# Performance work log

Hardware: AMD Instinct MI355X
Metric: run time of the kernel (lower is better)

The kernel has to match this reference:

```python
import jax, jax.numpy as jnp
import numpy as np

OUT_FEATURES = 4096
IN_FEATURES = 4096


def _unpack_int4_symmetric(packed, n_values):
    # packed: uint8-valued int32 array; each byte holds two 4-bit values:
    # high nibble first, low nibble second (packing was (v0 << 4) | v1 with v in [0,15]=q+8)
    high = (packed >> 4) & 15
    low = packed & 15
    interleaved = jnp.stack([high, low], axis=-1).reshape(-1)[:n_values]
    # symmetric: quantized value q = nibble - 8, zero_point = 0
    return interleaved.astype(jnp.float32) - 8.0


def setup_inputs() -> dict:
    key = jax.random.key(0)
    k1, k2, k3, k4, k5 = jax.random.split(key, 5)
    x = jax.random.normal(k1, (4, 2048, IN_FEATURES), dtype=jnp.float32)
    packed_w = jax.random.randint(k2, (OUT_FEATURES * IN_FEATURES // 2,), 0, 256, dtype=jnp.int32)
    packed_b = jax.random.randint(k3, (OUT_FEATURES // 2,), 0, 256, dtype=jnp.int32)
    scale_w = jax.random.uniform(k4, (), dtype=jnp.float32) * 0.01 + 1e-4
    scale_b = jax.random.uniform(k5, (), dtype=jnp.float32) * 0.01 + 1e-4
    return {"x": x, "packed_w": packed_w, "packed_b": packed_b,
            "scale_w": scale_w, "scale_b": scale_b}


def reference(x, packed_w, packed_b, scale_w, scale_b):
    # dequantize weight: scale * (q - zero_point), zero_point = 0 (symmetric)
    qw = _unpack_int4_symmetric(packed_w, OUT_FEATURES * IN_FEATURES)
    W = (scale_w * qw).reshape(OUT_FEATURES, IN_FEATURES)  # [O, I]
    qb = _unpack_int4_symmetric(packed_b, OUT_FEATURES)
    b = scale_b * qb  # [O]
    # F.linear(x, W, b) = x @ W.T + b
    return jnp.einsum('bsi,oi->bso', x, W) + b
```

## Files before the change

kernel.cpp:

```cpp
#include <hip/hip_runtime.h>
#include <hip/hip_bf16.h>

#define M_DIM 8192
#define N_DIM 4096
#define K_DIM 4096

typedef _Float16 f16;
typedef _Float16 f16x8 __attribute__((ext_vector_type(8)));
typedef float f32x16 __attribute__((ext_vector_type(16)));

__device__ __forceinline__ void lds_async16(void* lds, const void* g) {
    __builtin_amdgcn_global_load_lds(
        (const __attribute__((address_space(1))) void*)(void*)g,
        (__attribute__((address_space(3))) void*)lds, 16, 0, 0);
}

__global__ __launch_bounds__(256) void cvt_x_kernel(const float* __restrict__ x, f16* __restrict__ xh) {
    size_t idx  = (size_t)blockIdx.x * 256 + threadIdx.x;
    size_t base = idx * 8;
    const float4* xp = (const float4*)(x + base);
    float4 v0 = xp[0], v1 = xp[1];
    f16x8 h;
    h[0] = (f16)v0.x; h[1] = (f16)v0.y; h[2] = (f16)v0.z; h[3] = (f16)v0.w;
    h[4] = (f16)v1.x; h[5] = (f16)v1.y; h[6] = (f16)v1.z; h[7] = (f16)v1.w;
    *(f16x8*)(xh + base) = h;
}

__global__ __launch_bounds__(256) void cvt_w_kernel(const int* __restrict__ pw, f16* __restrict__ wh) {
    size_t idx = (size_t)blockIdx.x * 256 + threadIdx.x;
    int4 v = ((const int4*)pw)[idx];
    f16x8 h;
    int a;
    a = v.x; h[0] = (f16)(((a >> 4) & 15) - 8); h[1] = (f16)((a & 15) - 8);
    a = v.y; h[2] = (f16)(((a >> 4) & 15) - 8); h[3] = (f16)((a & 15) - 8);
    a = v.z; h[4] = (f16)(((a >> 4) & 15) - 8); h[5] = (f16)((a & 15) - 8);
    a = v.w; h[6] = (f16)(((a >> 4) & 15) - 8); h[7] = (f16)((a & 15) - 8);
    *(f16x8*)(wh + idx * 8) = h;
}

__global__ __launch_bounds__(256) void gemm_f16(const f16* __restrict__ A, const f16* __restrict__ B,
                                                const int* __restrict__ pb,
                                                const float* __restrict__ psw, const float* __restrict__ psb,
                                                float* __restrict__ out) {
    __shared__ f16 As[128 * 64];
    __shared__ f16 Bs[128 * 64];

    const int tid  = threadIdx.x;
    const int wave = tid >> 6;
    const int lane = tid & 63;
    const int wm   = wave >> 1;
    const int wn   = wave & 1;
    const int half = lane >> 5;
    const int l32  = lane & 31;

    const int mbase = blockIdx.y * 128;
    const int nbase = blockIdx.x * 128;

    const int srow = lane >> 3;
    const int scol = ((lane & 7) ^ srow) * 8;

    const f16* aP[4]; const f16* bP[4];
    f16* aD[4]; f16* bD[4];
#pragma unroll
    for (int j = 0; j < 4; j++) {
        aP[j] = A + (size_t)(mbase + wave * 32 + j * 8 + srow) * K_DIM + scol;
        bP[j] = B + (size_t)(nbase + wave * 32 + j * 8 + srow) * K_DIM + scol;
        aD[j] = As + (wave * 4 + j) * 512;
        bD[j] = Bs + (wave * 4 + j) * 512;
    }

    f32x16 acc[2][2] = {};

    int abase[2], bbase[2], arr[2], brr[2];
#pragma unroll
    for (int t = 0; t < 2; t++) {
        int ra = wm * 64 + t * 32 + l32;
        int rb = wn * 64 + t * 32 + l32;
        abase[t] = (ra >> 3) * 512 + (ra & 7) * 64;
        arr[t]   = ra & 7;
        bbase[t] = (rb >> 3) * 512 + (rb & 7) * 64;
        brr[t]   = rb & 7;
    }

    for (int k0 = 0; k0 < K_DIM; k0 += 64) {
#pragma unroll
        for (int j = 0; j < 4; j++) {
            lds_async16(aD[j], aP[j]);
            lds_async16(bD[j], bP[j]);
            aP[j] += 64; bP[j] += 64;
        }
        __syncthreads();

#pragma unroll
        for (int kk = 0; kk < 64; kk += 16) {
            const int kc = (kk >> 3) + half;
            f16x8 af[2], bf[2];
#pragma unroll
            for (int t = 0; t < 2; t++) {
                af[t] = *(const f16x8*)&As[abase[t] + (kc ^ arr[t]) * 8];
                bf[t] = *(const f16x8*)&Bs[bbase[t] + (kc ^ brr[t]) * 8];
            }
#pragma unroll
            for (int mt = 0; mt < 2; mt++)
#pragma unroll
                for (int nt = 0; nt < 2; nt++)
                    acc[mt][nt] = __builtin_amdgcn_mfma_f32_32x32x16_f16(af[mt], bf[nt], acc[mt][nt], 0, 0, 0);
        }

        __syncthreads();
    }

    const float sw = *psw;
    const float sb = *psb;

#pragma unroll
    for (int nt = 0; nt < 2; nt++) {
        const int gcol = nbase + wn * 64 + nt * 32 + l32;
        const int p    = pb[gcol >> 1];
        const int nib  = (gcol & 1) ? (p & 15) : ((p >> 4) & 15);
        const float bias = sb * (float)(nib - 8);
#pragma unroll
        for (int mt = 0; mt < 2; mt++) {
            const int rbase = mbase + wm * 64 + mt * 32 + half * 4;
#pragma unroll
            for (int g = 0; g < 4; g++) {
                float* o = out + (size_t)(rbase + g * 8) * N_DIM + gcol;
#pragma unroll
                for (int r = 0; r < 4; r++)
                    o[(size_t)r * N_DIM] = sw * acc[mt][nt][g * 4 + r] + bias;
            }
        }
    }
}

__global__ __launch_bounds__(256) void gemm_fallback(const float* __restrict__ x, const int* __restrict__ pw,
                                                     const int* __restrict__ pb,
                                                     const float* __restrict__ psw, const float* __restrict__ psb,
                                                     float* __restrict__ out) {
    __shared__ float As[16][17];
    __shared__ float Bs[16][17];
    const int tx = threadIdx.x & 15, ty = threadIdx.x >> 4;
    const int row = blockIdx.y * 16 + ty;
    const int col = blockIdx.x * 16 + tx;
    float acc = 0.f;
    for (int k0 = 0; k0 < K_DIM; k0 += 16) {
        As[ty][tx] = x[(size_t)row * K_DIM + k0 + tx];
        const int nrow = blockIdx.x * 16 + ty;
        const int k = k0 + tx;
        const int p = pw[((size_t)nrow * K_DIM + k) >> 1];
        const int nib = (k & 1) ? (p & 15) : ((p >> 4) & 15);
        Bs[ty][tx] = (float)(nib - 8);
        __syncthreads();
#pragma unroll
        for (int kk = 0; kk < 16; kk++)
            acc += As[ty][kk] * Bs[tx][kk];
        __syncthreads();
    }
    const float sw = *psw, sb = *psb;
    const int p = pb[col >> 1];
    const int nib = (col & 1) ? (p & 15) : ((p >> 4) & 15);
    out[(size_t)row * N_DIM + col] = sw * acc + sb * (float)(nib - 8);
}

extern "C" void kernel_launch(void* const* d_in, const int* in_sizes, int n_in,
                              void* d_out, int out_size, void* d_ws, size_t ws_size,
                              hipStream_t stream) {
    (void)in_sizes; (void)n_in; (void)out_size;
    const float* x   = (const float*)d_in[0];
    const int*   pw  = (const int*)d_in[1];
    const int*   pb  = (const int*)d_in[2];
    const float* psw = (const float*)d_in[3];
    const float* psb = (const float*)d_in[4];
    float* out = (float*)d_out;

    const size_t xh_bytes = (size_t)M_DIM * K_DIM * sizeof(f16);
    const size_t wh_bytes = (size_t)N_DIM * K_DIM * sizeof(f16);

    if (ws_size >= xh_bytes + wh_bytes) {
        f16* xh = (f16*)d_ws;
        f16* wh = (f16*)((char*)d_ws + xh_bytes);
        cvt_x_kernel<<<(M_DIM * (size_t)K_DIM) / 8 / 256, 256, 0, stream>>>(x, xh);
        cvt_w_kernel<<<((size_t)N_DIM * K_DIM / 2) / 4 / 256, 256, 0, stream>>>(pw, wh);
        gemm_f16<<<dim3(N_DIM / 128, M_DIM / 128), 256, 0, stream>>>(xh, wh, pb, psw, psb, out);
    } else {
        gemm_fallback<<<dim3(N_DIM / 16, M_DIM / 16), 256, 0, stream>>>(x, pw, pb, psw, psb, out);
    }
}
```

Baseline: 504.6 us.

## Rewrite GEMM as 256x256 tile, 8-wave, double-buffered pipelined MFMA kernel

The f16 GEMM moves from 128x128 tiles with 4 waves and a load-then-sync loop to 256x256 tiles with 8 waves. LDS is double-buffered and the K-loop is split into four phases that interleave async global-to-LDS loads with MFMA work, using explicit barriers, waitcnt and setprio. It also adds block-index swizzling for L2 locality and a new LDS XOR swizzle. The goal is to hide load latency and raise data reuse per tile, at the cost of more LDS and registers per block and fragile hand-written synchronisation.

```diff
diff --git a/kernel.cpp b/kernel.cpp
--- a/kernel.cpp
+++ b/kernel.cpp
@@ -1,5 +1,4 @@
 #include <hip/hip_runtime.h>
-#include <hip/hip_bf16.h>
 
 #define M_DIM 8192
 #define N_DIM 4096
@@ -38,77 +37,120 @@
     *(f16x8*)(wh + idx * 8) = h;
 }
 
-__global__ __launch_bounds__(256) void gemm_f16(const f16* __restrict__ A, const f16* __restrict__ B,
-                                                const int* __restrict__ pb,
-                                                const float* __restrict__ psw, const float* __restrict__ psb,
-                                                float* __restrict__ out) {
-    __shared__ f16 As[128 * 64];
-    __shared__ f16 Bs[128 * 64];
+
+#define PHASE(AC, BC, KK, STAGE_STMT, VM_STMT) do {                                              \
+    const int h_   = (KK) >> 1;                                                                  \
+    const int kc2_ = ((KK) & 1) * 2 + half;                                                      \
+    f16x8 af0 = *(const f16x8*)&(AC)[h_ * 8192 + aoff[0] + ((kc2_ ^ axr[0]) << 3)];              \
+    f16x8 af1 = *(const f16x8*)&(AC)[h_ * 8192 + aoff[1] + ((kc2_ ^ axr[1]) << 3)];              \
+    f16x8 af2 = *(const f16x8*)&(AC)[h_ * 8192 + aoff[2] + ((kc2_ ^ axr[2]) << 3)];              \
+    f16x8 af3 = *(const f16x8*)&(AC)[h_ * 8192 + aoff[3] + ((kc2_ ^ axr[3]) << 3)];              \
+    f16x8 bf0 = *(const f16x8*)&(BC)[h_ * 8192 + boff[0] + ((kc2_ ^ bxr[0]) << 3)];              \
+    f16x8 bf1 = *(const f16x8*)&(BC)[h_ * 8192 + boff[1] + ((kc2_ ^ bxr[1]) << 3)];              \
+    STAGE_STMT;                                                                                  \
+    __builtin_amdgcn_s_barrier();                                                                \
+    asm volatile("s_waitcnt lgkmcnt(0)" ::: "memory");                                           \
+    __builtin_amdgcn_sched_barrier(0);                                                           \
+    __builtin_amdgcn_s_setprio(1);                                                               \
+    acc[0][0] = __builtin_amdgcn_mfma_f32_32x32x16_f16(af0, bf0, acc[0][0], 0, 0, 0);            \
+    acc[0][1] = __builtin_amdgcn_mfma_f32_32x32x16_f16(af0, bf1, acc[0][1], 0, 0, 0);            \
+    acc[1][0] = __builtin_amdgcn_mfma_f32_32x32x16_f16(af1, bf0, acc[1][0], 0, 0, 0);            \
+    acc[1][1] = __builtin_amdgcn_mfma_f32_32x32x16_f16(af1, bf1, acc[1][1], 0, 0, 0);            \
+    acc[2][0] = __builtin_amdgcn_mfma_f32_32x32x16_f16(af2, bf0, acc[2][0], 0, 0, 0);            \
+    acc[2][1] = __builtin_amdgcn_mfma_f32_32x32x16_f16(af2, bf1, acc[2][1], 0, 0, 0);            \
+    acc[3][0] = __builtin_amdgcn_mfma_f32_32x32x16_f16(af3, bf0, acc[3][0], 0, 0, 0);            \
+    acc[3][1] = __builtin_amdgcn_mfma_f32_32x32x16_f16(af3, bf1, acc[3][1], 0, 0, 0);            \
+    __builtin_amdgcn_s_setprio(0);                                                               \
+    VM_STMT;                                                                                     \
+    __builtin_amdgcn_s_barrier();                                                                \
+} while (0)
+
+#define TILE_STEP(AC, BC, AN, BN, T) do {                                                        \
+    const int kn_ = ((T) < 63) ? ((T) + 1) * 64 : 63 * 64;   \
+    PHASE(AC, BC, 0,                                                                             \
+          { lds_async16(&(AN)[dA0], aSrc[0] + kn_); lds_async16(&(AN)[dA1], aSrc[1] + kn_); },   \
+          );                                                                                     \
+    PHASE(AC, BC, 1,                                                                             \
+          { lds_async16(&(BN)[dA0], bSrc[0] + kn_); lds_async16(&(BN)[dA1], bSrc[1] + kn_); },   \
+          asm volatile("s_waitcnt vmcnt(4)" ::: "memory"));                                      \
+    PHASE(AC, BC, 2,                                                                             \
+          { lds_async16(&(AN)[8192 + dA0], aSrc[0] + kn_ + 32);                                  \
+            lds_async16(&(AN)[8192 + dA1], aSrc[1] + kn_ + 32); },                               \
+          );                                                                                     \
+    PHASE(AC, BC, 3,                                                                             \
+          { lds_async16(&(BN)[8192 + dA0], bSrc[0] + kn_ + 32);                                  \
+            lds_async16(&(BN)[8192 + dA1], bSrc[1] + kn_ + 32); },                               \
+          asm volatile("s_waitcnt vmcnt(4)" ::: "memory"));                                      \
+} while (0)
+
+__global__ __launch_bounds__(512, 2) void gemm_f16(const f16* __restrict__ A, const f16* __restrict__ B,
+                                                   const int* __restrict__ pb,
+                                                   const float* __restrict__ psw, const float* __restrict__ psb,
+                                                   float* __restrict__ out) {
+    __shared__ f16 As[2][16384];
+    __shared__ f16 Bs[2][16384];
 
     const int tid  = threadIdx.x;
     const int wave = tid >> 6;
     const int lane = tid & 63;
-    const int wm   = wave >> 1;
-    const int wn   = wave & 1;
+    const int l32  = lane & 31;
     const int half = lane >> 5;
-    const int l32  = lane & 31;
-
-    const int mbase = blockIdx.y * 128;
-    const int nbase = blockIdx.x * 128;
-
-    const int srow = lane >> 3;
-    const int scol = ((lane & 7) ^ srow) * 8;
-
-    const f16* aP[4]; const f16* bP[4];
-    f16* aD[4]; f16* bD[4];
-#pragma unroll
-    for (int j = 0; j < 4; j++) {
-        aP[j] = A + (size_t)(mbase + wave * 32 + j * 8 + srow) * K_DIM + scol;
-        bP[j] = B + (size_t)(nbase + wave * 32 + j * 8 + srow) * K_DIM + scol;
-        aD[j] = As + (wave * 4 + j) * 512;
-        bD[j] = Bs + (wave * 4 + j) * 512;
-    }
-
-    f32x16 acc[2][2] = {};
-
-    int abase[2], bbase[2], arr[2], brr[2];
-#pragma unroll
-    for (int t = 0; t < 2; t++) {
-        int ra = wm * 64 + t * 32 + l32;
-        int rb = wn * 64 + t * 32 + l32;
-        abase[t] = (ra >> 3) * 512 + (ra & 7) * 64;
-        arr[t]   = ra & 7;
-        bbase[t] = (rb >> 3) * 512 + (rb & 7) * 64;
-        brr[t]   = rb & 7;
-    }
-
-    for (int k0 = 0; k0 < K_DIM; k0 += 64) {
-#pragma unroll
-        for (int j = 0; j < 4; j++) {
-            lds_async16(aD[j], aP[j]);
-            lds_async16(bD[j], bP[j]);
-            aP[j] += 64; bP[j] += 64;
-        }
-        __syncthreads();
-
-#pragma unroll
-        for (int kk = 0; kk < 64; kk += 16) {
-            const int kc = (kk >> 3) + half;
-            f16x8 af[2], bf[2];
-#pragma unroll
-            for (int t = 0; t < 2; t++) {
-                af[t] = *(const f16x8*)&As[abase[t] + (kc ^ arr[t]) * 8];
-                bf[t] = *(const f16x8*)&Bs[bbase[t] + (kc ^ brr[t]) * 8];
-            }
-#pragma unroll
-            for (int mt = 0; mt < 2; mt++)
-#pragma unroll
-                for (int nt = 0; nt < 2; nt++)
-                    acc[mt][nt] = __builtin_amdgcn_mfma_f32_32x32x16_f16(af[mt], bf[nt], acc[mt][nt], 0, 0, 0);
-        }
-
-        __syncthreads();
-    }
+    const int wm   = wave >> 2;
+    const int wn   = wave & 3;
+
+    const int bid = blockIdx.x;
+    const int swz = (bid & 7) * 64 + (bid >> 3);
+    const int bx  = swz & 15;
+    const int by  = swz >> 4;
+    const int mbase = by * 256;
+    const int nbase = bx * 256;
+
+    const int rL   = ((lane >> 5) & 1) * 8 + ((lane >> 2) & 7);
+    const int kswz = (((lane & 3) ^ ((lane >> 3) & 3))) * 8;
+    const f16* aSrc[2]; const f16* bSrc[2];
+#pragma unroll
+    for (int j = 0; j < 2; j++) {
+        aSrc[j] = A + (size_t)(mbase + j * 128 + wave * 16 + rL) * K_DIM + kswz;
+        bSrc[j] = B + (size_t)(nbase + j * 128 + wave * 16 + rL) * K_DIM + kswz;
+    }
+    const int dA0 = wave * 512;
+    const int dA1 = 4096 + wave * 512;
+
+    int aoff[4], axr[4];
+#pragma unroll
+    for (int mt = 0; mt < 4; mt++) {
+        int ra = wm * 128 + mt * 32 + l32;
+        aoff[mt] = (ra >> 3) * 256 + (ra & 7) * 32;
+        axr[mt]  = ((ra & 7) >> 1) & 3;
+    }
+    int boff[2], bxr[2];
+#pragma unroll
+    for (int nt = 0; nt < 2; nt++) {
+        int rb = wn * 64 + nt * 32 + l32;
+        boff[nt] = (rb >> 3) * 256 + (rb & 7) * 32;
+        bxr[nt]  = ((rb & 7) >> 1) & 3;
+    }
+
+    f32x16 acc[4][2] = {};
+
+    lds_async16(&As[0][dA0], aSrc[0]);
+    lds_async16(&As[0][dA1], aSrc[1]);
+    lds_async16(&Bs[0][dA0], bSrc[0]);
+    lds_async16(&Bs[0][dA1], bSrc[1]);
+    lds_async16(&As[0][8192 + dA0], aSrc[0] + 32);
+    lds_async16(&As[0][8192 + dA1], aSrc[1] + 32);
+    lds_async16(&Bs[0][8192 + dA0], bSrc[0] + 32);
+    lds_async16(&Bs[0][8192 + dA1], bSrc[1] + 32);
+    asm volatile("s_waitcnt vmcnt(4)" ::: "memory");
+    __builtin_amdgcn_s_barrier();
+
+#pragma unroll 1
+    for (int t = 0; t < 64; t += 2) {
+        TILE_STEP(As[0], Bs[0], As[1], Bs[1], t);
+        TILE_STEP(As[1], Bs[1], As[0], Bs[0], t + 1);
+    }
+
+    asm volatile("s_waitcnt vmcnt(0)" ::: "memory");
 
     const float sw = *psw;
     const float sb = *psb;
@@ -120,8 +162,8 @@
         const int nib  = (gcol & 1) ? (p & 15) : ((p >> 4) & 15);
         const float bias = sb * (float)(nib - 8);
 #pragma unroll
-        for (int mt = 0; mt < 2; mt++) {
-            const int rbase = mbase + wm * 64 + mt * 32 + half * 4;
+        for (int mt = 0; mt < 4; mt++) {
+            const int rbase = mbase + wm * 128 + mt * 32 + half * 4;
 #pragma unroll
             for (int g = 0; g < 4; g++) {
                 float* o = out + (size_t)(rbase + g * 8) * N_DIM + gcol;
@@ -181,7 +223,7 @@
         f16* wh = (f16*)((char*)d_ws + xh_bytes);
         cvt_x_kernel<<<(M_DIM * (size_t)K_DIM) / 8 / 256, 256, 0, stream>>>(x, xh);
         cvt_w_kernel<<<((size_t)N_DIM * K_DIM / 2) / 4 / 256, 256, 0, stream>>>(pw, wh);
-        gemm_f16<<<dim3(N_DIM / 128, M_DIM / 128), 256, 0, stream>>>(xh, wh, pb, psw, psb, out);
+        gemm_f16<<<dim3((M_DIM / 256) * (N_DIM / 256)), 512, 0, stream>>>(xh, wh, pb, psw, psb, out);
     } else {
         gemm_fallback<<<dim3(N_DIM / 16, M_DIM / 16), 256, 0, stream>>>(x, pw, pb, psw, psb, out);
     }
```

Result: slower. 536.8 us (+6.4%).

## Fuse fp32-to-fp16 X conversion into GEMM with double-buffered B and tile swizzle

Applied to the files above, without the earlier changes.

Drops the separate pass that converted X to fp16. The GEMM now loads fp32 X directly, converts it in registers and writes it to LDS. The B tile is double-buffered with async global-to-LDS loads issued one step ahead, the grid is flattened with a block-index swizzle to improve L2 locality, and occupancy is hinted with launch_bounds(256,3). This removes a full read and write of the 64MB X intermediate, but X is now read as fp32 per N-tile, doubling A-side traffic inside the GEMM, and the A loads are synchronous register loads rather than async.

```diff
diff --git a/kernel.cpp b/kernel.cpp
--- a/kernel.cpp
+++ b/kernel.cpp
@@ -1,5 +1,4 @@
 #include <hip/hip_runtime.h>
-#include <hip/hip_bf16.h>
 
 #define M_DIM 8192
 #define N_DIM 4096
@@ -13,17 +12,6 @@
     __builtin_amdgcn_global_load_lds(
         (const __attribute__((address_space(1))) void*)(void*)g,
         (__attribute__((address_space(3))) void*)lds, 16, 0, 0);
-}
-
-__global__ __launch_bounds__(256) void cvt_x_kernel(const float* __restrict__ x, f16* __restrict__ xh) {
-    size_t idx  = (size_t)blockIdx.x * 256 + threadIdx.x;
-    size_t base = idx * 8;
-    const float4* xp = (const float4*)(x + base);
-    float4 v0 = xp[0], v1 = xp[1];
-    f16x8 h;
-    h[0] = (f16)v0.x; h[1] = (f16)v0.y; h[2] = (f16)v0.z; h[3] = (f16)v0.w;
-    h[4] = (f16)v1.x; h[5] = (f16)v1.y; h[6] = (f16)v1.z; h[7] = (f16)v1.w;
-    *(f16x8*)(xh + base) = h;
 }
 
 __global__ __launch_bounds__(256) void cvt_w_kernel(const int* __restrict__ pw, f16* __restrict__ wh) {
@@ -38,12 +26,12 @@
     *(f16x8*)(wh + idx * 8) = h;
 }
 
-__global__ __launch_bounds__(256) void gemm_f16(const f16* __restrict__ A, const f16* __restrict__ B,
-                                                const int* __restrict__ pb,
-                                                const float* __restrict__ psw, const float* __restrict__ psb,
-                                                float* __restrict__ out) {
+__global__ __launch_bounds__(256, 3) void gemm_f16(const float* __restrict__ X, const f16* __restrict__ B,
+                                                   const int* __restrict__ pb,
+                                                   const float* __restrict__ psw, const float* __restrict__ psb,
+                                                   float* __restrict__ out) {
     __shared__ f16 As[128 * 64];
-    __shared__ f16 Bs[128 * 64];
+    __shared__ f16 Bs[2][128 * 64];
 
     const int tid  = threadIdx.x;
     const int wave = tid >> 6;
@@ -53,52 +41,80 @@
     const int half = lane >> 5;
     const int l32  = lane & 31;
 
-    const int mbase = blockIdx.y * 128;
-    const int nbase = blockIdx.x * 128;
+    const int bid = blockIdx.x;
+    const int swz = (bid & 7) * 256 + (bid >> 3);
+    const int bx  = swz & 31;
+    const int by  = swz >> 5;
+    const int mbase = by * 128;
+    const int nbase = bx * 128;
 
     const int srow = lane >> 3;
-    const int scol = ((lane & 7) ^ srow) * 8;
-
-    const f16* aP[4]; const f16* bP[4];
-    f16* aD[4]; f16* bD[4];
+    const int skc  = (lane & 7) ^ srow;
+
+    const float* aP[4]; const f16* bP[4]; f16* aD[4];
 #pragma unroll
     for (int j = 0; j < 4; j++) {
-        aP[j] = A + (size_t)(mbase + wave * 32 + j * 8 + srow) * K_DIM + scol;
-        bP[j] = B + (size_t)(nbase + wave * 32 + j * 8 + srow) * K_DIM + scol;
-        aD[j] = As + (wave * 4 + j) * 512;
-        bD[j] = Bs + (wave * 4 + j) * 512;
+        aP[j] = X + (size_t)(mbase + wave * 32 + j * 8 + srow) * K_DIM + skc * 8;
+        bP[j] = B + (size_t)(nbase + wave * 32 + j * 8 + srow) * K_DIM + skc * 8;
+        aD[j] = As + (wave * 4 + j) * 512 + lane * 8;
     }
 
     f32x16 acc[2][2] = {};
 
     int abase[2], bbase[2], arr[2], brr[2];
 #pragma unroll
-    for (int t = 0; t < 2; t++) {
-        int ra = wm * 64 + t * 32 + l32;
-        int rb = wn * 64 + t * 32 + l32;
-        abase[t] = (ra >> 3) * 512 + (ra & 7) * 64;
-        arr[t]   = ra & 7;
-        bbase[t] = (rb >> 3) * 512 + (rb & 7) * 64;
-        brr[t]   = rb & 7;
-    }
-
-    for (int k0 = 0; k0 < K_DIM; k0 += 64) {
+    for (int tt = 0; tt < 2; tt++) {
+        int ra = wm * 64 + tt * 32 + l32;
+        int rb = wn * 64 + tt * 32 + l32;
+        abase[tt] = (ra >> 3) * 512 + (ra & 7) * 64;
+        arr[tt]   = ra & 7;
+        bbase[tt] = (rb >> 3) * 512 + (rb & 7) * 64;
+        brr[tt]   = rb & 7;
+    }
+
+#pragma unroll
+    for (int j = 0; j < 4; j++)
+        lds_async16(&Bs[0][(wave * 4 + j) * 512], bP[j]);
+
+#pragma unroll 1
+    for (int t = 0; t < 64; ++t) {
+        const int koff = t * 64;
+
+        float4 va[4][2];
 #pragma unroll
         for (int j = 0; j < 4; j++) {
-            lds_async16(aD[j], aP[j]);
-            lds_async16(bD[j], bP[j]);
-            aP[j] += 64; bP[j] += 64;
-        }
-        __syncthreads();
-
-#pragma unroll
-        for (int kk = 0; kk < 64; kk += 16) {
-            const int kc = (kk >> 3) + half;
+            const float4* p = (const float4*)(aP[j] + koff);
+            va[j][0] = p[0]; va[j][1] = p[1];
+        }
+#pragma unroll
+        for (int j = 0; j < 4; j++) {
+            f16x8 h;
+            h[0] = (f16)va[j][0].x; h[1] = (f16)va[j][0].y; h[2] = (f16)va[j][0].z; h[3] = (f16)va[j][0].w;
+            h[4] = (f16)va[j][1].x; h[5] = (f16)va[j][1].y; h[6] = (f16)va[j][1].z; h[7] = (f16)va[j][1].w;
+            *(f16x8*)aD[j] = h;
+        }
+        {
+            const int kn = (t < 63 ? t + 1 : 63) * 64;
+            f16* bN = &Bs[(t + 1) & 1][0];
+#pragma unroll
+            for (int j = 0; j < 4; j++)
+                lds_async16(bN + (wave * 4 + j) * 512, bP[j] + kn);
+        }
+        asm volatile("s_waitcnt vmcnt(4)" ::: "memory");
+        asm volatile("s_waitcnt lgkmcnt(0)" ::: "memory");
+        __builtin_amdgcn_sched_barrier(0);
+        __builtin_amdgcn_s_barrier();
+        __builtin_amdgcn_sched_barrier(0);
+
+        const f16* bC = &Bs[t & 1][0];
+#pragma unroll
+        for (int kk = 0; kk < 4; ++kk) {
+            const int kc = kk * 2 + half;
             f16x8 af[2], bf[2];
 #pragma unroll
-            for (int t = 0; t < 2; t++) {
-                af[t] = *(const f16x8*)&As[abase[t] + (kc ^ arr[t]) * 8];
-                bf[t] = *(const f16x8*)&Bs[bbase[t] + (kc ^ brr[t]) * 8];
+            for (int tt = 0; tt < 2; tt++) {
+                af[tt] = *(const f16x8*)&As[abase[tt] + ((kc ^ arr[tt])) * 8];
+                bf[tt] = *(const f16x8*)&bC[bbase[tt] + ((kc ^ brr[tt])) * 8];
             }
 #pragma unroll
             for (int mt = 0; mt < 2; mt++)
@@ -107,8 +123,11 @@
                     acc[mt][nt] = __builtin_amdgcn_mfma_f32_32x32x16_f16(af[mt], bf[nt], acc[mt][nt], 0, 0, 0);
         }
 
-        __syncthreads();
-    }
+        __builtin_amdgcn_s_barrier();
+        __builtin_amdgcn_sched_barrier(0);
+    }
+
+    asm volatile("s_waitcnt vmcnt(0)" ::: "memory");
 
     const float sw = *psw;
     const float sb = *psb;
@@ -173,15 +192,12 @@
     const float* psb = (const float*)d_in[4];
     float* out = (float*)d_out;
 
-    const size_t xh_bytes = (size_t)M_DIM * K_DIM * sizeof(f16);
     const size_t wh_bytes = (size_t)N_DIM * K_DIM * sizeof(f16);
 
-    if (ws_size >= xh_bytes + wh_bytes) {
-        f16* xh = (f16*)d_ws;
-        f16* wh = (f16*)((char*)d_ws + xh_bytes);
-        cvt_x_kernel<<<(M_DIM * (size_t)K_DIM) / 8 / 256, 256, 0, stream>>>(x, xh);
+    if (ws_size >= wh_bytes) {
+        f16* wh = (f16*)d_ws;
         cvt_w_kernel<<<((size_t)N_DIM * K_DIM / 2) / 4 / 256, 256, 0, stream>>>(pw, wh);
-        gemm_f16<<<dim3(N_DIM / 128, M_DIM / 128), 256, 0, stream>>>(xh, wh, pb, psw, psb, out);
+        gemm_f16<<<dim3((N_DIM / 128) * (M_DIM / 128)), 256, 0, stream>>>(x, wh, pb, psw, psb, out);
     } else {
         gemm_fallback<<<dim3(N_DIM / 16, M_DIM / 16), 256, 0, stream>>>(x, pw, pb, psw, psb, out);
     }
```

Measured after the change: 621.8 us. 23.2% more time.
